# Kernel tuning notes

Measured on AMD Instinct MI355X. Metric: run time of the kernel, lower is better.

The kernel has to match this reference:

```python
import jax, jax.numpy as jnp
import numpy as np
import math

B, T, C, H = 2, 2048, 1024, 16
D = C // H  # head dim = 64
ROPE_BASE = 10000.0


def _rope(x):
    # x: (B, T, H, D); interleaved-pair RoPE matching torch apply_rope
    theta = jnp.exp(jnp.arange(0, D, 2, dtype=jnp.float32) * (-math.log(ROPE_BASE) / D))  # (D/2,)
    ang = jnp.arange(T, dtype=jnp.float32)[:, None] * theta[None, :]  # (T, D/2)
    cos = jnp.cos(ang)[None, :, None, :]  # (1, T, 1, D/2)
    sin = jnp.sin(ang)[None, :, None, :]
    xr = x.reshape(B, T, H, D // 2, 2)
    x0, x1 = xr[..., 0], xr[..., 1]
    out = jnp.stack([x0 * cos - x1 * sin, x1 * cos + x0 * sin], axis=-1)
    return out.reshape(B, T, H, D).astype(x.dtype)


def setup_inputs() -> dict:
    key = jax.random.key(0)
    k0, k1, k2 = jax.random.split(key, 3)
    x = jax.random.normal(k0, (B, T, C), dtype=jnp.float32)
    Wqkv = jax.random.normal(k1, (3 * C, C), dtype=jnp.float32) * 0.02
    bqkv = jnp.zeros((3 * C,), dtype=jnp.float32)
    Wproj = jax.random.normal(k2, (C, C), dtype=jnp.float32) * 0.02
    bproj = jnp.zeros((C,), dtype=jnp.float32)
    return {"x": x, "Wqkv": Wqkv, "bqkv": bqkv, "Wproj": Wproj, "bproj": bproj}


def reference(x, Wqkv, bqkv, Wproj, bproj):
    qkv = x @ Wqkv.T + bqkv  # (B, T, 3C)
    q, k, v = jnp.split(qkv, 3, axis=-1)
    q = _rope(q.reshape(B, T, H, D)).transpose(0, 2, 1, 3)  # (B, H, T, D)
    k = _rope(k.reshape(B, T, H, D)).transpose(0, 2, 1, 3)
    v = v.reshape(B, T, H, D).transpose(0, 2, 1, 3)
    scores = jnp.einsum('bhqd,bhkd->bhqk', q, k) * (1.0 / math.sqrt(D))
    causal = jnp.tril(jnp.ones((T, T), dtype=bool))  # (T, T)
    scores = jnp.where(causal[None, None, :, :], scores, -jnp.inf)
    attn = jax.nn.softmax(scores, axis=-1)
    y = jnp.einsum('bhqk,bhkd->bhqd', attn, v)  # (B, H, T, D)
    y = y.transpose(0, 2, 1, 3).reshape(B, T, C)
    return y @ Wproj.T + bproj
```

## Files before the change

### kernel.cpp

```cpp
#include <hip/hip_runtime.h>

typedef unsigned short u16;
typedef unsigned int u32;
typedef __bf16 bf16x8 __attribute__((ext_vector_type(8)));
typedef float f32x4 __attribute__((ext_vector_type(4)));
typedef float f32x16 __attribute__((ext_vector_type(16)));

#define BB 2
#define TT 2048
#define CC 1024
#define HH 16
#define DD 64
#define MR (BB*TT)
#define NQ (3*CC)
#define SCQ 0.18033688f

__device__ __forceinline__ u16 f2b(float f) {
    u32 u = __builtin_bit_cast(u32, f);
    u = (u + 0x7fffu + ((u >> 16) & 1u)) >> 16;
    return (u16)u;
}
__device__ __forceinline__ float b2f(u16 b) {
    return __builtin_bit_cast(float, (u32)b << 16);
}
__device__ __forceinline__ u32 pkbf(float a, float b) {
    ushort2 t; t.x = f2b(a); t.y = f2b(b);
    return __builtin_bit_cast(u32, t);
}

__device__ __forceinline__ void gll16(const void* g, void* l) {
    __builtin_amdgcn_global_load_lds(
        (const __attribute__((address_space(1))) void*)g,
        (__attribute__((address_space(3))) void*)l,
        16, 0, 0);
}

__global__ void cvt_all(const float* __restrict__ x, const float* __restrict__ wqkv,
                        const float* __restrict__ wproj,
                        u16* __restrict__ xb, u16* __restrict__ wqkvb, u16* __restrict__ wprojb,
                        u32* __restrict__ ctr)
{
    if (blockIdx.x == 0 && threadIdx.x == 0) *ctr = 0;
    const int n0 = MR * CC / 4, n1 = NQ * CC / 4, n2 = CC * CC / 4;
    int i = blockIdx.x * 256 + threadIdx.x;
    const float* src; u16* dst; int off;
    if (i < n0)           { src = x;     dst = xb;     off = i; }
    else if (i < n0 + n1) { src = wqkv;  dst = wqkvb;  off = i - n0; }
    else if (i < n0 + n1 + n2) { src = wproj; dst = wprojb; off = i - n0 - n1; }
    else return;
    float4 v = reinterpret_cast<const float4*>(src)[off];
    ushort4 o;
    o.x = f2b(v.x); o.y = f2b(v.y); o.z = f2b(v.z); o.w = f2b(v.w);
    reinterpret_cast<ushort4*>(dst)[off] = o;
}

template<int BF16_OUT>
__global__ __launch_bounds__(256) void gemm_bt(
    const u16* __restrict__ A, const u16* __restrict__ Bm,
    const float* __restrict__ bias, void* __restrict__ outp,
    int M, int N, int K)
{
    __shared__ __align__(16) u16 As[128 * 32];
    __shared__ __align__(16) u16 Bs[128 * 32];
    const int tid = threadIdx.x;
    const int lane = tid & 63;
    const int w = tid >> 6;
    const int wr = w >> 1, wc = w & 1;
    const int fr = lane & 15, fq = lane >> 4;
    const int brow = blockIdx.y * 128, bcol = blockIdx.x * 128;
    const int srow = lane >> 2;
    const int scol = (lane & 3) * 8;

    f32x4 acc[4][4];
    const f32x4 zero = {0.f, 0.f, 0.f, 0.f};
#pragma unroll
    for (int i = 0; i < 4; i++)
#pragma unroll
        for (int j = 0; j < 4; j++) acc[i][j] = zero;

    for (int kt = 0; kt < K; kt += 32) {
#pragma unroll
        for (int i = 0; i < 2; i++) {
            const int r = i * 64 + w * 16 + srow;
            gll16(&A[(size_t)(brow + r) * K + kt + scol], &As[(i * 64 + w * 16) * 32]);
            gll16(&Bm[(size_t)(bcol + r) * K + kt + scol], &Bs[(i * 64 + w * 16) * 32]);
        }
        __syncthreads();
        bf16x8 af[4], bfr[4];
#pragma unroll
        for (int mi = 0; mi < 4; mi++)
            af[mi] = *reinterpret_cast<const bf16x8*>(&As[(wr * 64 + mi * 16 + fr) * 32 + fq * 8]);
#pragma unroll
        for (int nj = 0; nj < 4; nj++)
            bfr[nj] = *reinterpret_cast<const bf16x8*>(&Bs[(wc * 64 + nj * 16 + fr) * 32 + fq * 8]);
#pragma unroll
        for (int mi = 0; mi < 4; mi++)
#pragma unroll
            for (int nj = 0; nj < 4; nj++)
                acc[mi][nj] = __builtin_amdgcn_mfma_f32_16x16x32_bf16(af[mi], bfr[nj], acc[mi][nj], 0, 0, 0);
        __syncthreads();
    }

#pragma unroll
    for (int mi = 0; mi < 4; mi++) {
#pragma unroll
        for (int nj = 0; nj < 4; nj++) {
            const int n = bcol + wc * 64 + nj * 16 + fr;
            const float bn = bias[n];
#pragma unroll
            for (int r = 0; r < 4; r++) {
                const int m = brow + wr * 64 + mi * 16 + fq * 4 + r;
                const float v = acc[mi][nj][r] + bn;
                if (BF16_OUT) reinterpret_cast<u16*>(outp)[(size_t)m * N + n] = f2b(v);
                else          reinterpret_cast<float*>(outp)[(size_t)m * N + n] = v;
            }
        }
    }
}

__global__ void rope_reorder(const u16* __restrict__ qkv,
                             u16* __restrict__ Qr, u16* __restrict__ Kr)
{
    const int idx = blockIdx.x * 256 + threadIdx.x;
    const int j = idx & 31;
    const int h = (idx >> 5) & 15;
    const int t = (idx >> 9) & 2047;
    const int b = idx >> 20;
    const size_t mrow = (size_t)(b * TT + t) * NQ;
    const float theta = __expf((float)(2 * j) * (-0.14391157f));
    const float ang = (float)t * theta;
    const float cs = cosf(ang), sn = sinf(ang);
    const int qc = h * DD + 2 * j;
    const float q0 = b2f(qkv[mrow + qc]),          q1 = b2f(qkv[mrow + qc + 1]);
    const float k0 = b2f(qkv[mrow + CC + qc]),     k1 = b2f(qkv[mrow + CC + qc + 1]);
    const size_t obase = ((size_t)(b * HH + h) * TT + t) * DD + 2 * j;
    Qr[obase]     = f2b((q0 * cs - q1 * sn) * SCQ);
    Qr[obase + 1] = f2b((q1 * cs + q0 * sn) * SCQ);
    Kr[obase]     = f2b(k0 * cs - k1 * sn);
    Kr[obase + 1] = f2b(k1 * cs + k0 * sn);
}

__global__ __launch_bounds__(64) void vtrans(const u16* __restrict__ qkv, u16* __restrict__ Vtg)
{
    const int lane = threadIdx.x;
    const int t0 = blockIdx.x * 64;
    const int bh = blockIdx.y;
    const int b = bh >> 4, h = bh & 15;
    u32 packed[32];
#pragma unroll
    for (int tt = 0; tt < 64; tt += 2) {
        const u16 a = qkv[(size_t)(b * TT + t0 + tt) * NQ + 2 * CC + h * DD + lane];
        const u16 c = qkv[(size_t)(b * TT + t0 + tt + 1) * NQ + 2 * CC + h * DD + lane];
        packed[tt >> 1] = (u32)a | ((u32)c << 16);
    }
    u32* dst = reinterpret_cast<u32*>(&Vtg[((size_t)bh * DD + lane) * TT + t0]);
#pragma unroll
    for (int i = 0; i < 32; i += 4)
        *reinterpret_cast<uint4*>(&dst[i]) = make_uint4(packed[i], packed[i + 1], packed[i + 2], packed[i + 3]);
}

__global__ __launch_bounds__(512) void attn_fwd(
    const u16* __restrict__ Q, const u16* __restrict__ Kg, const u16* __restrict__ Vtg,
    u16* __restrict__ Y, u32* __restrict__ ctr)
{
    __shared__ __align__(16) u16 smem[4 * 64 * 72];
    __shared__ int cur;
    const int tid = threadIdx.x;
    const int lane = tid & 63;
    const int ql = lane & 31;
    const int hB = lane >> 5;
    const int wq = (tid >> 6) & 3;
    const int g  = tid >> 8;
    const int srow = (tid & 255) >> 2;
    const int sc   = tid & 3;
    u16* KsG = smem + (g * 2 + 0) * 4608;
    u16* VsG = smem + (g * 2 + 1) * 4608;
    float* fm = reinterpret_cast<float*>(smem);

    while (true) {
        if (tid == 0) cur = atomicAdd(ctr, 1);
        __syncthreads();
        const int it = cur;
        __syncthreads();
        if (it >= 512) break;

        const int bx = 15 - (it >> 5);
        const int bh = it & 31;
        const int q0 = bx << 7;
        const int halfL = bx + 1;
        const int b = bh >> 4, hh = bh & 15;
        const int qb = q0 + wq * 32;
        const int qg = qb + ql;
        const size_t base  = (size_t)bh * TT * DD;
        const size_t vbase = (size_t)bh * DD * TT;

        bf16x8 qf[4];
#pragma unroll
        for (int ds = 0; ds < 4; ds++)
            qf[ds] = *reinterpret_cast<const bf16x8*>(&Q[base + (size_t)qg * DD + ds * 16 + hB * 8]);

        f32x16 acc[2];
#pragma unroll
        for (int dh = 0; dh < 2; dh++)
#pragma unroll
            for (int r = 0; r < 16; r++) acc[dh][r] = 0.f;
        float m_ = -1e30f, l_ = 0.f;

        int kv0 = 64 * g;
        uint4 kr0, kr1, vr0, vr1;
        {
            const size_t kro = base + (size_t)(kv0 + srow) * DD;
            kr0 = *reinterpret_cast<const uint4*>(&Kg[kro + sc * 8]);
            kr1 = *reinterpret_cast<const uint4*>(&Kg[kro + 32 + sc * 8]);
            const size_t vro = vbase + (size_t)srow * TT + kv0;
            vr0 = *reinterpret_cast<const uint4*>(&Vtg[vro + sc * 8]);
            vr1 = *reinterpret_cast<const uint4*>(&Vtg[vro + 32 + sc * 8]);
        }

        for (int i = 0; i < halfL; ++i) {
            *reinterpret_cast<uint4*>(&KsG[srow * 72 + sc * 8])      = kr0;
            *reinterpret_cast<uint4*>(&KsG[srow * 72 + 32 + sc * 8]) = kr1;
            *reinterpret_cast<uint4*>(&VsG[srow * 72 + sc * 8])      = vr0;
            *reinterpret_cast<uint4*>(&VsG[srow * 72 + 32 + sc * 8]) = vr1;
            if (i + 1 < halfL) {
                const size_t kro = base + (size_t)(kv0 + 128 + srow) * DD;
                kr0 = *reinterpret_cast<const uint4*>(&Kg[kro + sc * 8]);
                kr1 = *reinterpret_cast<const uint4*>(&Kg[kro + 32 + sc * 8]);
                const size_t vro = vbase + (size_t)srow * TT + kv0 + 128;
                vr0 = *reinterpret_cast<const uint4*>(&Vtg[vro + sc * 8]);
                vr1 = *reinterpret_cast<const uint4*>(&Vtg[vro + 32 + sc * 8]);
            }
            __syncthreads();

            if (kv0 <= qb + 31) {
                f32x16 sa[2];
#pragma unroll
                for (int st = 0; st < 2; st++)
#pragma unroll
                    for (int r = 0; r < 16; r++) sa[st][r] = 0.f;
                __builtin_amdgcn_s_setprio(1);
#pragma unroll
                for (int st = 0; st < 2; st++)
#pragma unroll
                    for (int ds = 0; ds < 4; ds++) {
                        bf16x8 kf = *reinterpret_cast<const bf16x8*>(
                            &KsG[(st * 32 + ql) * 72 + ds * 16 + hB * 8]);
                        sa[st] = __builtin_amdgcn_mfma_f32_32x32x16_bf16(kf, qf[ds], sa[st], 0, 0, 0);
                    }
                __builtin_amdgcn_s_setprio(0);
                if (kv0 + 63 > qb) {
#pragma unroll
                    for (int st = 0; st < 2; st++) {
                        const int kb0 = kv0 + st * 32 + 4 * hB;
#pragma unroll
                        for (int r = 0; r < 16; r++) {
                            const int kg = kb0 + (r & 3) + 8 * (r >> 2);
                            if (kg > qg) sa[st][r] = -1e30f;
                        }
                    }
                }
                float mx[16];
#pragma unroll
                for (int j = 0; j < 16; j++) mx[j] = fmaxf(sa[0][j], sa[1][j]);
#pragma unroll
                for (int j = 0; j < 8; j++) mx[j] = fmaxf(mx[j], mx[j + 8]);
#pragma unroll
                for (int j = 0; j < 4; j++) mx[j] = fmaxf(mx[j], mx[j + 4]);
                float tm = fmaxf(fmaxf(mx[0], mx[1]), fmaxf(mx[2], mx[3]));
                tm = fmaxf(tm, __shfl_xor(tm, 32));
                const float mn = fmaxf(m_, tm);
                const bool need = __any(mn > m_);
                float scl = 1.0f;
                if (need) { scl = exp2f(m_ - mn); m_ = mn; }
#pragma unroll
                for (int st = 0; st < 2; st++)
#pragma unroll
                    for (int r = 0; r < 16; r++)
                        sa[st][r] = exp2f(sa[st][r] - m_);
                float ps[16];
#pragma unroll
                for (int j = 0; j < 16; j++) ps[j] = sa[0][j] + sa[1][j];
#pragma unroll
                for (int j = 0; j < 8; j++) ps[j] += ps[j + 8];
#pragma unroll
                for (int j = 0; j < 4; j++) ps[j] += ps[j + 4];
                float rs = (ps[0] + ps[1]) + (ps[2] + ps[3]);
                rs += __shfl_xor(rs, 32);
                if (need) {
                    l_ = l_ * scl + rs;
#pragma unroll
                    for (int dh = 0; dh < 2; dh++)
#pragma unroll
                        for (int r = 0; r < 16; r++) acc[dh][r] *= scl;
                } else {
                    l_ += rs;
                }
                u32 pk[2][8];
#pragma unroll
                for (int st = 0; st < 2; st++)
#pragma unroll
                    for (int wd = 0; wd < 8; wd++)
                        pk[st][wd] = pkbf(sa[st][2 * wd], sa[st][2 * wd + 1]);
                __builtin_amdgcn_s_setprio(1);
#pragma unroll
                for (int c = 0; c < 4; c++) {
                    u32 a0 = pk[c >> 1][4 * (c & 1) + 0];
                    u32 a1 = pk[c >> 1][4 * (c & 1) + 1];
                    u32 a2 = pk[c >> 1][4 * (c & 1) + 2];
                    u32 a3 = pk[c >> 1][4 * (c & 1) + 3];
                    asm volatile("v_permlane32_swap_b32 %0, %1" : "+v"(a0), "+v"(a2));
                    asm volatile("v_permlane32_swap_b32 %0, %1" : "+v"(a1), "+v"(a3));
                    uint4 tw = make_uint4(a0, a1, a2, a3);
                    bf16x8 pb = __builtin_bit_cast(bf16x8, tw);
#pragma unroll
                    for (int dh = 0; dh < 2; dh++) {
                        bf16x8 vf = *reinterpret_cast<const bf16x8*>(
                            &VsG[(dh * 32 + ql) * 72 + c * 16 + hB * 8]);
                        acc[dh] = __builtin_amdgcn_mfma_f32_32x32x16_bf16(vf, pb, acc[dh], 0, 0, 0);
                    }
                }
                __builtin_amdgcn_s_setprio(0);
            }
            __syncthreads();
            kv0 += 128;
        }

        const int fidx = (wq * 64 + lane) * 36;
        if (g == 1) {
#pragma unroll
            for (int dh = 0; dh < 2; dh++)
#pragma unroll
                for (int r = 0; r < 16; r++) fm[fidx + dh * 16 + r] = acc[dh][r];
            fm[fidx + 32] = m_;
            fm[fidx + 33] = l_;
        }
        __syncthreads();
        float o_sc1 = 0.f, o_sc2 = 0.f, linv = 0.f;
        float acc2[32];
        if (g == 0) {
            const float m2 = fm[fidx + 32];
            const float l2 = fm[fidx + 33];
            const float mm = fmaxf(m_, m2);
            o_sc1 = exp2f(m_ - mm);
            o_sc2 = exp2f(m2 - mm);
            const float lt = l_ * o_sc1 + l2 * o_sc2;
            linv = 1.0f / lt;
#pragma unroll
            for (int dh = 0; dh < 2; dh++)
#pragma unroll
                for (int r = 0; r < 16; r++) acc2[dh * 16 + r] = fm[fidx + dh * 16 + r];
        }
        __syncthreads();
        if (g == 0) {
            const int lrow = wq * 32 + ql;
#pragma unroll
            for (int dh = 0; dh < 2; dh++)
#pragma unroll
                for (int rp = 0; rp < 16; rp += 2) {
                    const int d = (rp & 3) + 8 * (rp >> 2) + 4 * hB + 32 * dh;
                    const float v0 = (acc[dh][rp]     * o_sc1 + acc2[dh * 16 + rp]     * o_sc2) * linv;
                    const float v1 = (acc[dh][rp + 1] * o_sc1 + acc2[dh * 16 + rp + 1] * o_sc2) * linv;
                    *reinterpret_cast<u32*>(&smem[lrow * 72 + d]) = pkbf(v0, v1);
                }
        }
        __syncthreads();
        {
            const int row = tid >> 2;
            const int ch = tid & 3;
#pragma unroll
            for (int p = 0; p < 2; ++p) {
                uint4 ov = *reinterpret_cast<const uint4*>(&smem[row * 72 + (ch + 4 * p) * 8]);
                *reinterpret_cast<uint4*>(&Y[(size_t)(b * TT + q0 + row) * CC + hh * DD + (ch + 4 * p) * 8]) = ov;
            }
        }
        __syncthreads();
    }
}

extern "C" void kernel_launch(void* const* d_in, const int* in_sizes, int n_in,
                              void* d_out, int out_size, void* d_ws, size_t ws_size,
                              hipStream_t stream)
{
    const float* x     = (const float*)d_in[0];
    const float* Wqkv  = (const float*)d_in[1];
    const float* bqkv  = (const float*)d_in[2];
    const float* Wproj = (const float*)d_in[3];
    const float* bproj = (const float*)d_in[4];
    float* out = (float*)d_out;

    u16* ws     = (u16*)d_ws;
    u16* xb     = ws;
    u16* wqkvb  = xb     + (size_t)MR * CC;
    u16* wprojb = wqkvb  + (size_t)NQ * CC;
    u16* qkv    = wprojb + (size_t)CC * CC;
    u16* Qr     = qkv    + (size_t)MR * NQ;
    u16* Kr     = Qr     + (size_t)BB * HH * TT * DD;
    u16* Vtg    = Kr     + (size_t)BB * HH * TT * DD;
    u16* yb     = Vtg    + (size_t)BB * HH * TT * DD;
    u32* ctr    = (u32*)(yb + (size_t)MR * CC);

    cvt_all<<<dim3(8192), 256, 0, stream>>>(x, Wqkv, Wproj, xb, wqkvb, wprojb, ctr);

    gemm_bt<1><<<dim3(NQ / 128, MR / 128), 256, 0, stream>>>(xb, wqkvb, bqkv, qkv, MR, NQ, CC);

    rope_reorder<<<dim3(BB * TT * HH * 32 / 256), 256, 0, stream>>>(qkv, Qr, Kr);
    vtrans<<<dim3(TT / 64, BB * HH), 64, 0, stream>>>(qkv, Vtg);

    attn_fwd<<<dim3(256), 512, 0, stream>>>(Qr, Kr, Vtg, yb, ctr);

    gemm_bt<0><<<dim3(CC / 128, MR / 128), 256, 0, stream>>>(yb, wprojb, bproj, out, MR, CC, CC);
}
```

Before: 217.7 us.

## Fuse RoPE and Q/K head reorder into QKV GEMM epilogue with precomputed table

Adds a dedicated QKV GEMM whose epilogue applies bias and RoPE, using a lane shuffle to fetch the pair partner, and writes Q/K directly in head-major layout while V goes to a compact buffer. This removes the separate rope_reorder kernel and the full qkv round-trip through memory. The cos/sin table is now computed once in the conversion kernel, and the block order is remapped for cache locality. The cost is scattered epilogue stores and table loads inside the GEMM.

```diff
diff --git a/kernel.cpp b/kernel.cpp
--- a/kernel.cpp
+++ b/kernel.cpp
@@ -38,20 +38,110 @@
 __global__ void cvt_all(const float* __restrict__ x, const float* __restrict__ wqkv,
                         const float* __restrict__ wproj,
                         u16* __restrict__ xb, u16* __restrict__ wqkvb, u16* __restrict__ wprojb,
-                        u32* __restrict__ ctr)
+                        float2* __restrict__ tab, u32* __restrict__ ctr)
 {
     if (blockIdx.x == 0 && threadIdx.x == 0) *ctr = 0;
     const int n0 = MR * CC / 4, n1 = NQ * CC / 4, n2 = CC * CC / 4;
     int i = blockIdx.x * 256 + threadIdx.x;
-    const float* src; u16* dst; int off;
-    if (i < n0)           { src = x;     dst = xb;     off = i; }
-    else if (i < n0 + n1) { src = wqkv;  dst = wqkvb;  off = i - n0; }
-    else if (i < n0 + n1 + n2) { src = wproj; dst = wprojb; off = i - n0 - n1; }
-    else return;
-    float4 v = reinterpret_cast<const float4*>(src)[off];
-    ushort4 o;
-    o.x = f2b(v.x); o.y = f2b(v.y); o.z = f2b(v.z); o.w = f2b(v.w);
-    reinterpret_cast<ushort4*>(dst)[off] = o;
+    if (i < n0 + n1 + n2) {
+        const float* src; u16* dst; int off;
+        if (i < n0)           { src = x;     dst = xb;     off = i; }
+        else if (i < n0 + n1) { src = wqkv;  dst = wqkvb;  off = i - n0; }
+        else                  { src = wproj; dst = wprojb; off = i - n0 - n1; }
+        float4 v = reinterpret_cast<const float4*>(src)[off];
+        ushort4 o;
+        o.x = f2b(v.x); o.y = f2b(v.y); o.z = f2b(v.z); o.w = f2b(v.w);
+        reinterpret_cast<ushort4*>(dst)[off] = o;
+    } else {
+        const int e = i - (n0 + n1 + n2);
+        if (e < TT * 32) {
+            const int t = e >> 5, j = e & 31;
+            const float theta = expf((float)(2 * j) * (-0.14391157f));
+            float s, c;
+            sincosf((float)t * theta, &s, &c);
+            tab[e] = make_float2(c, s);
+        }
+    }
+}
+
+__global__ __launch_bounds__(256) void gemm_qkv(
+    const u16* __restrict__ A, const u16* __restrict__ Bm,
+    const float* __restrict__ bias, const float2* __restrict__ tab,
+    u16* __restrict__ Qr, u16* __restrict__ Kr, u16* __restrict__ Vc)
+{
+    __shared__ __align__(16) u16 As[128 * 32];
+    __shared__ __align__(16) u16 Bs[128 * 32];
+    const int K = CC;
+    const int tid = threadIdx.x;
+    const int lane = tid & 63;
+    const int w = tid >> 6;
+    const int wr = w >> 1, wc = w & 1;
+    const int fr = lane & 15, fq = lane >> 4;
+    const int orig = blockIdx.y * 24 + blockIdx.x;
+    const int wg = (orig & 7) * 96 + (orig >> 3);
+    const int brow = (wg / 24) * 128, bcol = (wg % 24) * 128;
+    const int srow = lane >> 2;
+    const int scol = (lane & 3) * 8;
+
+    f32x4 acc[4][4];
+    const f32x4 zero = {0.f, 0.f, 0.f, 0.f};
+#pragma unroll
+    for (int i = 0; i < 4; i++)
+#pragma unroll
+        for (int j = 0; j < 4; j++) acc[i][j] = zero;
+
+    for (int kt = 0; kt < K; kt += 32) {
+#pragma unroll
+        for (int i = 0; i < 2; i++) {
+            const int r = i * 64 + w * 16 + srow;
+            gll16(&A[(size_t)(brow + r) * K + kt + scol], &As[(i * 64 + w * 16) * 32]);
+            gll16(&Bm[(size_t)(bcol + r) * K + kt + scol], &Bs[(i * 64 + w * 16) * 32]);
+        }
+        __syncthreads();
+        bf16x8 af[4], bfr[4];
+#pragma unroll
+        for (int mi = 0; mi < 4; mi++)
+            af[mi] = *reinterpret_cast<const bf16x8*>(&As[(wr * 64 + mi * 16 + fr) * 32 + fq * 8]);
+#pragma unroll
+        for (int nj = 0; nj < 4; nj++)
+            bfr[nj] = *reinterpret_cast<const bf16x8*>(&Bs[(wc * 64 + nj * 16 + fr) * 32 + fq * 8]);
+#pragma unroll
+        for (int mi = 0; mi < 4; mi++)
+#pragma unroll
+            for (int nj = 0; nj < 4; nj++)
+                acc[mi][nj] = __builtin_amdgcn_mfma_f32_16x16x32_bf16(af[mi], bfr[nj], acc[mi][nj], 0, 0, 0);
+        __syncthreads();
+    }
+
+#pragma unroll
+    for (int mi = 0; mi < 4; mi++) {
+#pragma unroll
+        for (int nj = 0; nj < 4; nj++) {
+            const int n = bcol + wc * 64 + nj * 16 + fr;
+            const float bn = bias[n];
+            const int sec = n >> 10;
+            const int h = (n >> 6) & 15;
+            const int d = n & 63;
+            const int j = d >> 1;
+            const bool odd = d & 1;
+#pragma unroll
+            for (int r = 0; r < 4; r++) {
+                const int m = brow + wr * 64 + mi * 16 + fq * 4 + r;
+                const int b = m >> 11, t = m & 2047;
+                const float v = acc[mi][nj][r] + bn;
+                const float p = __shfl_xor(v, 1);
+                if (sec == 2) {
+                    Vc[(size_t)m * CC + (n - 2 * CC)] = f2b(v);
+                } else {
+                    const float2 cs = tab[t * 32 + j];
+                    const float o = odd ? (v * cs.x + p * cs.y) : (v * cs.x - p * cs.y);
+                    const size_t oidx = ((size_t)(b * HH + h) * TT + t) * DD + d;
+                    if (sec == 0) Qr[oidx] = f2b(o * SCQ);
+                    else          Kr[oidx] = f2b(o);
+                }
+            }
+        }
+    }
 }
 
 template<int BF16_OUT>
@@ -118,29 +208,7 @@
     }
 }
 
-__global__ void rope_reorder(const u16* __restrict__ qkv,
-                             u16* __restrict__ Qr, u16* __restrict__ Kr)
-{
-    const int idx = blockIdx.x * 256 + threadIdx.x;
-    const int j = idx & 31;
-    const int h = (idx >> 5) & 15;
-    const int t = (idx >> 9) & 2047;
-    const int b = idx >> 20;
-    const size_t mrow = (size_t)(b * TT + t) * NQ;
-    const float theta = __expf((float)(2 * j) * (-0.14391157f));
-    const float ang = (float)t * theta;
-    const float cs = cosf(ang), sn = sinf(ang);
-    const int qc = h * DD + 2 * j;
-    const float q0 = b2f(qkv[mrow + qc]),          q1 = b2f(qkv[mrow + qc + 1]);
-    const float k0 = b2f(qkv[mrow + CC + qc]),     k1 = b2f(qkv[mrow + CC + qc + 1]);
-    const size_t obase = ((size_t)(b * HH + h) * TT + t) * DD + 2 * j;
-    Qr[obase]     = f2b((q0 * cs - q1 * sn) * SCQ);
-    Qr[obase + 1] = f2b((q1 * cs + q0 * sn) * SCQ);
-    Kr[obase]     = f2b(k0 * cs - k1 * sn);
-    Kr[obase + 1] = f2b(k1 * cs + k0 * sn);
-}
-
-__global__ __launch_bounds__(64) void vtrans(const u16* __restrict__ qkv, u16* __restrict__ Vtg)
+__global__ __launch_bounds__(64) void vtrans(const u16* __restrict__ Vc, u16* __restrict__ Vtg)
 {
     const int lane = threadIdx.x;
     const int t0 = blockIdx.x * 64;
@@ -149,8 +217,8 @@
     u32 packed[32];
 #pragma unroll
     for (int tt = 0; tt < 64; tt += 2) {
-        const u16 a = qkv[(size_t)(b * TT + t0 + tt) * NQ + 2 * CC + h * DD + lane];
-        const u16 c = qkv[(size_t)(b * TT + t0 + tt + 1) * NQ + 2 * CC + h * DD + lane];
+        const u16 a = Vc[(size_t)(b * TT + t0 + tt) * CC + h * DD + lane];
+        const u16 c = Vc[(size_t)(b * TT + t0 + tt + 1) * CC + h * DD + lane];
         packed[tt >> 1] = (u32)a | ((u32)c << 16);
     }
     u32* dst = reinterpret_cast<u32*>(&Vtg[((size_t)bh * DD + lane) * TT + t0]);
@@ -392,19 +460,19 @@
     u16* xb     = ws;
     u16* wqkvb  = xb     + (size_t)MR * CC;
     u16* wprojb = wqkvb  + (size_t)NQ * CC;
-    u16* qkv    = wprojb + (size_t)CC * CC;
-    u16* Qr     = qkv    + (size_t)MR * NQ;
+    u16* Vc     = wprojb + (size_t)CC * CC;
+    u16* Qr     = Vc     + (size_t)MR * CC;
     u16* Kr     = Qr     + (size_t)BB * HH * TT * DD;
     u16* Vtg    = Kr     + (size_t)BB * HH * TT * DD;
     u16* yb     = Vtg    + (size_t)BB * HH * TT * DD;
-    u32* ctr    = (u32*)(yb + (size_t)MR * CC);
-
-    cvt_all<<<dim3(8192), 256, 0, stream>>>(x, Wqkv, Wproj, xb, wqkvb, wprojb, ctr);
-
-    gemm_bt<1><<<dim3(NQ / 128, MR / 128), 256, 0, stream>>>(xb, wqkvb, bqkv, qkv, MR, NQ, CC);
-
-    rope_reorder<<<dim3(BB * TT * HH * 32 / 256), 256, 0, stream>>>(qkv, Qr, Kr);
-    vtrans<<<dim3(TT / 64, BB * HH), 64, 0, stream>>>(qkv, Vtg);
+    float2* tab = (float2*)(yb + (size_t)MR * CC);
+    u32* ctr    = (u32*)(tab + (size_t)TT * 32);
+
+    cvt_all<<<dim3(8448), 256, 0, stream>>>(x, Wqkv, Wproj, xb, wqkvb, wprojb, tab, ctr);
+
+    gemm_qkv<<<dim3(24, 32), 256, 0, stream>>>(xb, wqkvb, bqkv, tab, Qr, Kr, Vc);
+
+    vtrans<<<dim3(TT / 64, BB * HH), 64, 0, stream>>>(Vc, Vtg);
 
     attn_fwd<<<dim3(256), 512, 0, stream>>>(Qr, Kr, Vtg, yb, ctr);
 
```

Measured after the change: 212.7 us. 2.3% less time.
